# Kernel optimization log

Hardware: AMD Instinct MI355X
Metric: run time of the kernel (lower is better)

Reference implementation:

```python
import jax, jax.numpy as jnp
import numpy as np

B, L = 16, 8192
D, NB, N, NC = 128, 6, 32, 16   # d_model, n_blocks, complex state modes (d_state//2), num_classes
E = 2 * D                       # FF expansion (expand=2)


def setup_inputs() -> dict:
    key = jax.random.key(0)
    ks = jax.random.split(key, 16)
    rn = lambda k, s, sc=0.02: jax.random.normal(k, s, jnp.float32) * sc
    return {
        "x": jax.random.normal(ks[0], (B, L, 1), jnp.float32),
        "conv_w": rn(ks[1], (D, 1, 5), 0.3),
        "conv_b": jnp.zeros((D,), jnp.float32),
        "s4_ln_w": jnp.ones((NB, D), jnp.float32),
        "s4_ln_b": jnp.zeros((NB, D), jnp.float32),
        "s4_log_dt": jax.random.uniform(ks[2], (NB, D), jnp.float32, np.log(1e-3), np.log(1e-1)),
        "s4_log_A_real": jnp.full((NB, D, N), np.log(0.5), jnp.float32),
        "s4_A_imag": jnp.ones((NB, D, 1), jnp.float32) * (np.pi * jnp.arange(N, dtype=jnp.float32)),
        "s4_C_re": rn(ks[3], (NB, D, N), 1.0),
        "s4_C_im": rn(ks[4], (NB, D, N), 1.0),
        "s4_D": rn(ks[5], (NB, D), 1.0),
        "s4_out_w": rn(ks[6], (NB, 2 * D, D)),
        "s4_out_b": jnp.zeros((NB, 2 * D), jnp.float32),
        "ff_ln_w": jnp.ones((NB, D), jnp.float32),
        "ff_ln_b": jnp.zeros((NB, D), jnp.float32),
        "ff_w1": rn(ks[7], (NB, E, D)),
        "ff_b1": jnp.zeros((NB, E), jnp.float32),
        "ff_w2": rn(ks[8], (NB, D, E)),
        "ff_b2": jnp.zeros((NB, D), jnp.float32),
        "head_w": rn(ks[9], (NC, D)),
        "head_b": jnp.zeros((NC,), jnp.float32),
    }


def _ln_c(h, w, b):
    # LayerNorm over channel dim of [B, D, L] (prenorm of ResidualBlock, transposed layout)
    mu = h.mean(1, keepdims=True)
    var = ((h - mu) ** 2).mean(1, keepdims=True)
    return (h - mu) * jax.lax.rsqrt(var + 1e-5) * w[None, :, None] + b[None, :, None]


def _s4(z, log_dt, log_A_real, A_imag, C_re, C_im, Dskip, out_w, out_b):
    # S4D diagonal SSM: ZOH-discretized kernel, FFT causal conv, GELU, GLU output projection
    Lq = z.shape[-1]
    dt = jnp.exp(log_dt)                                 # [D]
    A = -jnp.exp(log_A_real) + 1j * A_imag               # [D,N] stable diagonal
    dtA = dt[:, None] * A                                # [D,N]
    C = (C_re + 1j * C_im) * (jnp.exp(dtA) - 1.0) / A    # ZOH input discretization folded into C
    vand = jnp.exp(dtA[:, :, None] * jnp.arange(Lq))     # [D,N,L] Vandermonde of exp(dtA)
    K = 2.0 * jnp.einsum('dn,dnl->dl', C, vand).real     # [D,L] SSM convolution kernel
    nf = 2 * Lq
    y = jnp.fft.irfft(jnp.fft.rfft(z, n=nf) * jnp.fft.rfft(K, n=nf)[None], n=nf)[..., :Lq]
    y = jax.nn.gelu(y + Dskip[None, :, None] * z)        # skip term D*u then activation
    y = jnp.einsum('ed,bdl->bel', out_w, y) + out_b[None, :, None]  # position-wise d->2d
    a, g = jnp.split(y, 2, axis=1)
    return a * jax.nn.sigmoid(g)                          # GLU


def _logits(x, conv_w, conv_b, s4_ln_w, s4_ln_b, s4_log_dt, s4_log_A_real, s4_A_imag, s4_C_re, s4_C_im, s4_D, s4_out_w, s4_out_b, ff_ln_w, ff_ln_b, ff_w1, ff_b1, ff_w2, ff_b2, head_w, head_b):
    u = x.transpose(0, 2, 1)                             # [B,1,L]
    h = jax.lax.conv_general_dilated(u, conv_w, (1,), [(2, 2)], dimension_numbers=('NCH', 'OIH', 'NCH'))
    h = h + conv_b[None, :, None]                        # [B,D,L]
    nb = s4_log_dt.shape[0]
    for i in range(nb):
        z = _ln_c(h, s4_ln_w[i], s4_ln_b[i])
        h = h + _s4(z, s4_log_dt[i], s4_log_A_real[i], s4_A_imag[i], s4_C_re[i], s4_C_im[i], s4_D[i], s4_out_w[i], s4_out_b[i])
        z = _ln_c(h, ff_ln_w[i], ff_ln_b[i])
        z = jax.nn.gelu(jnp.einsum('ed,bdl->bel', ff_w1[i], z) + ff_b1[i][None, :, None])
        h = h + jnp.einsum('de,bel->bdl', ff_w2[i], z) + ff_b2[i][None, :, None]
    last = h[:, :, -1]                                   # take final timestep
    return last @ head_w.T + head_b                      # [B,NC]


def reference(x, conv_w, conv_b, s4_ln_w, s4_ln_b, s4_log_dt, s4_log_A_real, s4_A_imag, s4_C_re, s4_C_im, s4_D, s4_out_w, s4_out_b, ff_ln_w, ff_ln_b, ff_w1, ff_b1, ff_w2, ff_b2, head_w, head_b):
    logits = _logits(x, conv_w, conv_b, s4_ln_w, s4_ln_b, s4_log_dt, s4_log_A_real, s4_A_imag, s4_C_re, s4_C_im, s4_D, s4_out_w, s4_out_b, ff_ln_w, ff_ln_b, ff_w1, ff_b1, ff_w2, ff_b2, head_w, head_b)
    return jnp.argmax(logits, axis=-1)[:, None].astype(jnp.int32)
```

## Files before the change

### kernel.cpp

```cpp
#include <hip/hip_runtime.h>
#include <math.h>

#define Bb 16
#define Ls 8192
#define Dm 128
#define NBK 6
#define Nst 32
#define NCl 16
#define Em 256
#define LC 128
#define NCH 64
#define BL (Bb*Ls)

typedef __attribute__((ext_vector_type(8))) short bfrag;
typedef __attribute__((ext_vector_type(4))) float f32x4;

__device__ __forceinline__ float geluf(float x) {
    float t = x * x;
    float g = x * fmaf(0.102952207f, t, 2.30234547f);
    float e = exp2f(-g);
    return x * __builtin_amdgcn_rcpf(1.f + e);
}
__device__ __forceinline__ float sigmf(float x) {
    return __builtin_amdgcn_rcpf(1.f + exp2f(-1.44269504f * x));
}

__device__ __forceinline__ unsigned short bf16r(float x) {
    unsigned u = __float_as_uint(x);
    return (unsigned short)((u + 0x7FFFu + ((u >> 16) & 1u)) >> 16);
}
__device__ __forceinline__ void split2(float x, unsigned short& h, unsigned short& l) {
    h = bf16r(x);
    float hf = __uint_as_float(((unsigned)h) << 16);
    l = bf16r(x - hf);
}

__global__ void s4e_conv(const float* __restrict__ x, const float* __restrict__ cw,
                         const float* __restrict__ cb, float* __restrict__ h) {
    int tid = blockIdx.x * 256 + threadIdx.x;
    int d4 = tid & 31;
    int t = tid >> 5;
    int l = t & (Ls - 1);
    int b = t >> 13;
    const float* xb = x + (size_t)b * Ls;
    float xs[5];
#pragma unroll
    for (int k = 0; k < 5; ++k) {
        int p = l + k - 2;
        xs[k] = (p >= 0 && p < Ls) ? xb[p] : 0.f;
    }
    float4 acc;
    float* ap = &acc.x;
#pragma unroll
    for (int j = 0; j < 4; ++j) {
        int d = d4 * 4 + j;
        float a = cb[d];
#pragma unroll
        for (int k = 0; k < 5; ++k) a = fmaf(cw[d * 5 + k], xs[k], a);
        ap[j] = a;
    }
    *(float4*)&h[(size_t)t * Dm + d4 * 4] = acc;
}

__global__ void s4e_lnstat(const float* __restrict__ h, float2* __restrict__ stats) {
    int tid = threadIdx.x;
    int t = blockIdx.x * 64 + (tid >> 2);
    int sub = tid & 3;
    const float* hp = h + (size_t)t * Dm + sub * 32;
    float s = 0.f, q = 0.f;
#pragma unroll
    for (int i = 0; i < 8; ++i) {
        float4 v = *(const float4*)(hp + i * 4);
        s += v.x + v.y + v.z + v.w;
        q += v.x * v.x + v.y * v.y + v.z * v.z + v.w * v.w;
    }
    s += __shfl_xor(s, 1); s += __shfl_xor(s, 2);
    q += __shfl_xor(q, 1); q += __shfl_xor(q, 2);
    float mu = s * (1.f / Dm);
    float rs = rsqrtf(q * (1.f / Dm) - mu * mu + 1e-5f);
    if (sub == 0) stats[t] = make_float2(mu, rs);
}

__global__ void s4e_setup6(const float* __restrict__ log_dt, const float* __restrict__ lAr,
                           const float* __restrict__ Aim, const float* __restrict__ Cre,
                           const float* __restrict__ Cim, float2* __restrict__ wv6,
                           float2* __restrict__ wp6, float2* __restrict__ Cc6) {
    int i = blockIdx.x;
    int d = threadIdx.x;
    const float* ld  = log_dt + i * Dm;
    const float* la  = lAr + i * Dm * Nst;
    const float* ai  = Aim + i * Dm * Nst;
    const float* cre = Cre + i * Dm * Nst;
    const float* cim = Cim + i * Dm * Nst;
    float2* wv = wv6 + i * (Nst * Dm);
    float2* wp = wp6 + i * (Nst * Dm);
    float2* Cc = Cc6 + i * (Nst * Dm);
    float dt = expf(ld[d]);
    for (int n = 0; n < Nst; ++n) {
        int id = d * Nst + n;
        float Ar = -expf(la[id]);
        float Ai = ai[id];
        float xr = dt * Ar, xi = dt * Ai;
        float er = expf(xr);
        float wr = er * cosf(xi), wi = er * sinf(xi);
        wv[n * Dm + d] = make_float2(wr, wi);
        float den = Ar * Ar + Ai * Ai;
        float inv = 1.f / den;
        float fr = ((wr - 1.f) * Ar + wi * Ai) * inv;
        float fi = (wi * Ar - (wr - 1.f) * Ai) * inv;
        Cc[n * Dm + d] = make_float2(2.f * (cre[id] * fr - cim[id] * fi),
                                     2.f * (cre[id] * fi + cim[id] * fr));
        float pr = wr, pi = wi;
#pragma unroll
        for (int sq = 0; sq < 7; ++sq) {
            float nr = pr * pr - pi * pi;
            float ni = 2.f * pr * pi;
            pr = nr; pi = ni;
        }
        wp[n * Dm + d] = make_float2(pr, pi);
    }
}

__global__ void s4e_wsplit6(const float* __restrict__ ow, const float* __restrict__ w1,
                            const float* __restrict__ w2, unsigned short* __restrict__ base0) {
    int idx = blockIdx.x * 256 + threadIdx.x;
    int layer = idx / 12288;
    int r = idx - layer * 12288;
    int mat = r >> 12;
    int g = r & 4095;
    int lane = g & 63;
    int fid = g >> 6;
    int col = lane & 15, q = lane >> 4;
    unsigned short* base = base0 + layer * 196608;
    const float* src;
    unsigned short *dh, *dl_;
    int rt, kt, K;
    if (mat == 0)      { src = ow + layer * 32768; K = 128; dh = base;          dl_ = base + 32768;  rt = fid >> 2; kt = fid & 3; }
    else if (mat == 1) { src = w1 + layer * 32768; K = 128; dh = base + 65536;  dl_ = base + 98304;  rt = fid >> 2; kt = fid & 3; }
    else               { src = w2 + layer * 32768; K = 256; dh = base + 131072; dl_ = base + 163840; rt = fid >> 3; kt = fid & 7; }
    int row = rt * 16 + col;
    int k0 = kt * 32 + q * 8;
    const float* sp = src + row * K + k0;
    bfrag vh, vl;
#pragma unroll
    for (int j = 0; j < 8; ++j) {
        unsigned short hh, ll;
        split2(sp[j], hh, ll);
        vh[j] = (short)hh; vl[j] = (short)ll;
    }
    *(bfrag*)&dh[g * 8] = vh;
    *(bfrag*)&dl_[g * 8] = vl;
}

__global__ __launch_bounds__(256) void s4e_s1(const float* __restrict__ h,
        const float2* __restrict__ stats, const float* __restrict__ lnw,
        const float* __restrict__ lnb, const float2* __restrict__ wv,
        float2* __restrict__ send) {
    __shared__ float2 stl[LC];
    int tid = threadIdx.x;
    int blk = blockIdx.x;
    int half = blk & 1;
    int chunk = blk >> 1;
    int c = chunk & (NCH - 1);
    int b = chunk >> 6;
    int dl = tid & 15;
    int m  = (tid >> 4) & 3;
    int dq = tid >> 6;
    int d  = half * 64 + dq * 16 + dl;
    int n0 = m * 8;
    if (tid < LC) stl[tid] = stats[(size_t)b * Ls + c * LC + tid];
    float wr[8], wi[8], sr[8], si[8];
#pragma unroll
    for (int k = 0; k < 8; ++k) {
        float2 t = wv[(n0 + k) * Dm + d];
        wr[k] = t.x; wi[k] = t.y; sr[k] = 0.f; si[k] = 0.f;
    }
    float wd = lnw[d], bd = lnb[d];
    const float* hp = h + ((size_t)b * Ls + c * LC) * Dm + d;
    __syncthreads();
#pragma unroll 1
    for (int j = 0; j < LC; j += 4) {
        float hv[4];
#pragma unroll
        for (int u = 0; u < 4; ++u) hv[u] = hp[(size_t)(j + u) * Dm];
        float zv[4];
#pragma unroll
        for (int u = 0; u < 4; ++u) {
            float2 sj = stl[j + u];
            zv[u] = (hv[u] - sj.x) * sj.y * wd + bd;
        }
#pragma unroll
        for (int u = 0; u < 4; ++u) {
            float z = zv[u];
#pragma unroll
            for (int k = 0; k < 8; ++k) {
                float t = fmaf(-wi[k], si[k], z);
                float nr = fmaf(wr[k], sr[k], t);
                float ni = fmaf(wi[k], sr[k], wr[k] * si[k]);
                sr[k] = nr; si[k] = ni;
            }
        }
    }
    float2* o = send + ((size_t)(b * NCH + c) * Nst + n0) * Dm + d;
#pragma unroll
    for (int k = 0; k < 8; ++k) o[k * Dm] = make_float2(sr[k], si[k]);
}

__global__ void s4e_s2(const float2* __restrict__ wp, float2* __restrict__ s) {
    int tid = blockIdx.x * 256 + threadIdx.x;
    int d = tid & 127;
    int n = (tid >> 7) & 31;
    int b = tid >> 12;
    float2 W = wp[n * Dm + d];
    float Sr = 0.f, Si = 0.f;
    size_t base = ((size_t)(b * NCH) * Nst + n) * Dm + d;
    size_t cs = (size_t)Nst * Dm;
    for (int c0 = 0; c0 < NCH; c0 += 8) {
        float2 E[8];
#pragma unroll
        for (int k = 0; k < 8; ++k) E[k] = s[base + (size_t)(c0 + k) * cs];
#pragma unroll
        for (int k = 0; k < 8; ++k) {
            float2 o = make_float2(Sr, Si);
            float nr = fmaf(W.x, Sr, fmaf(-W.y, Si, E[k].x));
            float ni = fmaf(W.x, Si, fmaf(W.y, Sr, E[k].y));
            Sr = nr; Si = ni;
            s[base + (size_t)(c0 + k) * cs] = o;
        }
    }
}

__global__ __launch_bounds__(256) void s4e_s3(const float* __restrict__ h,
        const float2* __restrict__ stats, const float* __restrict__ lnw,
        const float* __restrict__ lnb, const float2* __restrict__ wv,
        const float2* __restrict__ Cc, const float2* __restrict__ sinit,
        const float* __restrict__ Dsk,
        unsigned short* __restrict__ acth, unsigned short* __restrict__ actl) {
    __shared__ float2 stl[LC];
    int tid = threadIdx.x;
    int blk = blockIdx.x;
    int half = blk & 1;
    int chunk = blk >> 1;
    int c = chunk & (NCH - 1);
    int b = chunk >> 6;
    int dl = tid & 15;
    int m  = (tid >> 4) & 3;
    int dq = tid >> 6;
    int d  = half * 64 + dq * 16 + dl;
    int n0 = m * 8;
    if (tid < LC) stl[tid] = stats[(size_t)b * Ls + c * LC + tid];
    float wr[8], wi[8], cr[8], ci[8], sr[8], si[8];
    const float2* s0 = sinit + ((size_t)(b * NCH + c) * Nst + n0) * Dm + d;
#pragma unroll
    for (int k = 0; k < 8; ++k) {
        float2 t = wv[(n0 + k) * Dm + d];  wr[k] = t.x; wi[k] = t.y;
        float2 cc = Cc[(n0 + k) * Dm + d]; cr[k] = cc.x; ci[k] = cc.y;
        float2 ss = s0[k * Dm];            sr[k] = ss.x; si[k] = ss.y;
    }
    float wd = lnw[d], bd = lnb[d];
    float Dv = Dsk[d];
    size_t ib = ((size_t)b * Ls + c * LC) * Dm + d;
    __syncthreads();
#pragma unroll 1
    for (int j = 0; j < LC; j += 4) {
        float hv[4];
#pragma unroll
        for (int u = 0; u < 4; ++u) hv[u] = h[ib + (size_t)(j + u) * Dm];
        float zv[4];
#pragma unroll
        for (int u = 0; u < 4; ++u) {
            float2 sj = stl[j + u];
            zv[u] = (hv[u] - sj.x) * sj.y * wd + bd;
        }
#pragma unroll
        for (int u = 0; u < 4; ++u) {
            float z = zv[u];
            float acc = 0.f;
#pragma unroll
            for (int k = 0; k < 8; ++k) {
                float t = fmaf(-wi[k], si[k], z);
                float nr = fmaf(wr[k], sr[k], t);
                float ni = fmaf(wi[k], sr[k], wr[k] * si[k]);
                sr[k] = nr; si[k] = ni;
                acc = fmaf(cr[k], nr, acc);
                acc = fmaf(-ci[k], ni, acc);
            }
            acc += __shfl_xor(acc, 16);
            acc += __shfl_xor(acc, 32);
            if (m == 0) {
                float av = geluf(fmaf(Dv, z, acc));
                unsigned short hh, ll;
                split2(av, hh, ll);
                acth[ib + (size_t)(j + u) * Dm] = hh;
                actl[ib + (size_t)(j + u) * Dm] = ll;
            }
        }
    }
}

__global__ __launch_bounds__(256) void s4e_outproj(const unsigned short* __restrict__ acth,
        const unsigned short* __restrict__ actl, const unsigned short* __restrict__ wsp,
        const float* __restrict__ bias, float* __restrict__ h) {
    __shared__ __align__(16) unsigned short smem[8192];
    unsigned short* Ah = smem;
    unsigned short* Al = smem + 4096;
    float* Rf = (float*)smem;
    const unsigned short* Whi = wsp;
    const unsigned short* Wlo = wsp + 32768;
    size_t l0 = (size_t)blockIdx.x * 32;
    int tid = threadIdx.x;
    {
        const unsigned short* gh = acth + l0 * Dm;
        const unsigned short* gl = actl + l0 * Dm;
        for (int i = tid * 8; i < 32 * 128; i += 2048) {
            int r = i >> 7;
            int di = i ^ ((r & 7) << 3);
            *(bfrag*)&Ah[di] = *(const bfrag*)&gh[i];
            *(bfrag*)&Al[di] = *(const bfrag*)&gl[i];
        }
    }
    __syncthreads();
    int w = tid >> 6, lane = tid & 63;
    int col = lane & 15, q = lane >> 4;
    f32x4 acc[2][4];
#pragma unroll
    for (int m = 0; m < 2; ++m)
#pragma unroll
        for (int nt = 0; nt < 4; ++nt) acc[m][nt] = (f32x4){0.f, 0.f, 0.f, 0.f};
#pragma unroll
    for (int ks = 0; ks < 4; ++ks) {
        int kb = ks * 32 + q * 8;
        int i0 = (col * 128 + kb) ^ ((col & 7) << 3);
        int i1 = ((16 + col) * 128 + kb) ^ ((col & 7) << 3);
        bfrag a0h = *(bfrag*)&Ah[i0], a0l = *(bfrag*)&Al[i0];
        bfrag a1h = *(bfrag*)&Ah[i1], a1l = *(bfrag*)&Al[i1];
#pragma unroll
        for (int nt = 0; nt < 4; ++nt) {
            int rt = (nt < 2) ? (w * 2 + nt) : (8 + w * 2 + (nt - 2));
            int off = ((rt * 4 + ks) * 64 + lane) * 8;
            bfrag bh = *(const bfrag*)&Whi[off];
            bfrag bl = *(const bfrag*)&Wlo[off];
            acc[0][nt] = __builtin_amdgcn_mfma_f32_16x16x32_bf16(a0h, bh, acc[0][nt], 0, 0, 0);
            acc[0][nt] = __builtin_amdgcn_mfma_f32_16x16x32_bf16(a0h, bl, acc[0][nt], 0, 0, 0);
            acc[0][nt] = __builtin_amdgcn_mfma_f32_16x16x32_bf16(a0l, bh, acc[0][nt], 0, 0, 0);
            acc[1][nt] = __builtin_amdgcn_mfma_f32_16x16x32_bf16(a1h, bh, acc[1][nt], 0, 0, 0);
            acc[1][nt] = __builtin_amdgcn_mfma_f32_16x16x32_bf16(a1h, bl, acc[1][nt], 0, 0, 0);
            acc[1][nt] = __builtin_amdgcn_mfma_f32_16x16x32_bf16(a1l, bh, acc[1][nt], 0, 0, 0);
        }
    }
    __syncthreads();
#pragma unroll
    for (int m = 0; m < 2; ++m)
#pragma unroll
        for (int nt = 0; nt < 2; ++nt) {
            int dout = w * 32 + nt * 16 + col;
            float ba = bias[dout], bg = bias[dout + 128];
#pragma unroll
            for (int r = 0; r < 4; ++r) {
                int l = m * 16 + q * 4 + r;
                float a = acc[m][nt][r] + ba;
                float g = acc[m][nt + 2][r] + bg;
                Rf[l * 128 + dout] = a * sigmf(g);
            }
        }
    __syncthreads();
    size_t gb = l0 * Dm + (size_t)tid * 16;
#pragma unroll
    for (int i = 0; i < 4; ++i) {
        float4 r = *(float4*)&Rf[tid * 16 + i * 4];
        float4 hv = *(float4*)&h[gb + i * 4];
        hv.x += r.x; hv.y += r.y; hv.z += r.z; hv.w += r.w;
        *(float4*)&h[gb + i * 4] = hv;
    }
}

__global__ __launch_bounds__(256) void s4e_ffk(const float* __restrict__ lnw,
        const float* __restrict__ lnb, const unsigned short* __restrict__ wsp,
        const float* __restrict__ b1, const float* __restrict__ b2, float* __restrict__ h) {
    __shared__ __align__(16) unsigned short smem[24576];
    unsigned short* Zh = smem;
    unsigned short* Zl = smem + 4096;
    unsigned short* Eh = smem + 8192;
    unsigned short* El = smem + 16384;
    float* Rf = (float*)smem;
    const unsigned short* W1h = wsp + 65536;
    const unsigned short* W1l = wsp + 98304;
    const unsigned short* W2h = wsp + 131072;
    const unsigned short* W2l = wsp + 163840;
    size_t l0 = (size_t)blockIdx.x * 32;
    int tid = threadIdx.x;
    float hf[16];
    float s = 0.f, qq = 0.f;
    {
        const float* hp = h + l0 * Dm + (size_t)tid * 16;
#pragma unroll
        for (int i = 0; i < 4; ++i) {
            float4 v = *(const float4*)(hp + i * 4);
            hf[i * 4 + 0] = v.x; hf[i * 4 + 1] = v.y;
            hf[i * 4 + 2] = v.z; hf[i * 4 + 3] = v.w;
            s += v.x + v.y + v.z + v.w;
            qq += v.x * v.x + v.y * v.y + v.z * v.z + v.w * v.w;
        }
    }
    s  += __shfl_xor(s, 1);  s += __shfl_xor(s, 2);  s += __shfl_xor(s, 4);
    qq += __shfl_xor(qq, 1); qq += __shfl_xor(qq, 2); qq += __shfl_xor(qq, 4);
    float mu = s * (1.f / Dm);
    float rs = rsqrtf(qq * (1.f / Dm) - mu * mu + 1e-5f);
    int tok = tid >> 3, dc = (tid & 7) * 16;
#pragma unroll
    for (int g = 0; g < 2; ++g) {
        bfrag vh, vl;
#pragma unroll
        for (int k = 0; k < 8; ++k) {
            int d = dc + g * 8 + k;
            float v = (hf[g * 8 + k] - mu) * rs * lnw[d] + lnb[d];
            unsigned short hh, ll;
            split2(v, hh, ll);
            vh[k] = (short)hh; vl[k] = (short)ll;
        }
        int idx = (tok * 128 + dc + g * 8) ^ ((tok & 7) << 3);
        *(bfrag*)&Zh[idx] = vh;
        *(bfrag*)&Zl[idx] = vl;
    }
    __syncthreads();
    int w = tid >> 6, lane = tid & 63;
    int col = lane & 15, q = lane >> 4;
    f32x4 acc[2][4];
#pragma unroll
    for (int m = 0; m < 2; ++m)
#pragma unroll
        for (int nt = 0; nt < 4; ++nt) acc[m][nt] = (f32x4){0.f, 0.f, 0.f, 0.f};
#pragma unroll
    for (int ks = 0; ks < 4; ++ks) {
        int kb = ks * 32 + q * 8;
        int i0 = (col * 128 + kb) ^ ((col & 7) << 3);
        int i1 = ((16 + col) * 128 + kb) ^ ((col & 7) << 3);
        bfrag a0h = *(bfrag*)&Zh[i0], a0l = *(bfrag*)&Zl[i0];
        bfrag a1h = *(bfrag*)&Zh[i1], a1l = *(bfrag*)&Zl[i1];
#pragma unroll
        for (int nt = 0; nt < 4; ++nt) {
            int rt = w * 4 + nt;
            int off = ((rt * 4 + ks) * 64 + lane) * 8;
            bfrag bh = *(const bfrag*)&W1h[off];
            bfrag bl = *(const bfrag*)&W1l[off];
            acc[0][nt] = __builtin_amdgcn_mfma_f32_16x16x32_bf16(a0h, bh, acc[0][nt], 0, 0, 0);
            acc[0][nt] = __builtin_amdgcn_mfma_f32_16x16x32_bf16(a0h, bl, acc[0][nt], 0, 0, 0);
            acc[0][nt] = __builtin_amdgcn_mfma_f32_16x16x32_bf16(a0l, bh, acc[0][nt], 0, 0, 0);
            acc[1][nt] = __builtin_amdgcn_mfma_f32_16x16x32_bf16(a1h, bh, acc[1][nt], 0, 0, 0);
            acc[1][nt] = __builtin_amdgcn_mfma_f32_16x16x32_bf16(a1h, bl, acc[1][nt], 0, 0, 0);
            acc[1][nt] = __builtin_amdgcn_mfma_f32_16x16x32_bf16(a1l, bh, acc[1][nt], 0, 0, 0);
        }
    }
#pragma unroll
    for (int m = 0; m < 2; ++m)
#pragma unroll
        for (int nt = 0; nt < 4; ++nt) {
            int ei = w * 64 + nt * 16 + col;
            float bv = b1[ei];
#pragma unroll
            for (int r = 0; r < 4; ++r) {
                int l = m * 16 + q * 4 + r;
                float v = geluf(acc[m][nt][r] + bv);
                unsigned short hh, ll;
                split2(v, hh, ll);
                int idx = (l * 256 + ei) ^ ((l & 7) << 3);
                Eh[idx] = hh; El[idx] = ll;
            }
        }
    __syncthreads();
    f32x4 acc2[2][2];
#pragma unroll
    for (int m = 0; m < 2; ++m)
#pragma unroll
        for (int nt = 0; nt < 2; ++nt) acc2[m][nt] = (f32x4){0.f, 0.f, 0.f, 0.f};
#pragma unroll
    for (int ks = 0; ks < 8; ++ks) {
        int kb = ks * 32 + q * 8;
        int i0 = (col * 256 + kb) ^ ((col & 7) << 3);
        int i1 = ((16 + col) * 256 + kb) ^ ((col & 7) << 3);
        bfrag a0h = *(bfrag*)&Eh[i0], a0l = *(bfrag*)&El[i0];
        bfrag a1h = *(bfrag*)&Eh[i1], a1l = *(bfrag*)&El[i1];
#pragma unroll
        for (int nt = 0; nt < 2; ++nt) {
            int rt = w * 2 + nt;
            int off = ((rt * 8 + ks) * 64 + lane) * 8;
            bfrag bh = *(const bfrag*)&W2h[off];
            bfrag bl = *(const bfrag*)&W2l[off];
            acc2[0][nt] = __builtin_amdgcn_mfma_f32_16x16x32_bf16(a0h, bh, acc2[0][nt], 0, 0, 0);
            acc2[0][nt] = __builtin_amdgcn_mfma_f32_16x16x32_bf16(a0h, bl, acc2[0][nt], 0, 0, 0);
            acc2[0][nt] = __builtin_amdgcn_mfma_f32_16x16x32_bf16(a0l, bh, acc2[0][nt], 0, 0, 0);
            acc2[1][nt] = __builtin_amdgcn_mfma_f32_16x16x32_bf16(a1h, bh, acc2[1][nt], 0, 0, 0);
            acc2[1][nt] = __builtin_amdgcn_mfma_f32_16x16x32_bf16(a1h, bl, acc2[1][nt], 0, 0, 0);
            acc2[1][nt] = __builtin_amdgcn_mfma_f32_16x16x32_bf16(a1l, bh, acc2[1][nt], 0, 0, 0);
        }
    }
#pragma unroll
    for (int m = 0; m < 2; ++m)
#pragma unroll
        for (int nt = 0; nt < 2; ++nt) {
            int dout = w * 32 + nt * 16 + col;
            float bv = b2[dout];
#pragma unroll
            for (int r = 0; r < 4; ++r) {
                int l = m * 16 + q * 4 + r;
                Rf[l * 128 + dout] = acc2[m][nt][r] + bv;
            }
        }
    __syncthreads();
    size_t gb = l0 * Dm + (size_t)tid * 16;
#pragma unroll
    for (int i = 0; i < 4; ++i) {
        float4 r = *(float4*)&Rf[tid * 16 + i * 4];
        float4 o;
        o.x = hf[i * 4 + 0] + r.x; o.y = hf[i * 4 + 1] + r.y;
        o.z = hf[i * 4 + 2] + r.z; o.w = hf[i * 4 + 3] + r.w;
        *(float4*)&h[gb + i * 4] = o;
    }
}

__global__ void s4e_head(const float* __restrict__ h, const float* __restrict__ hw,
                         const float* __restrict__ hb, int* __restrict__ out) {
    __shared__ float logit[Bb][NCl];
    int tid = threadIdx.x;
    int b = tid >> 4, c = tid & 15;
    const float* hp = h + ((size_t)b * Ls + (Ls - 1)) * Dm;
    float acc = hb[c];
    for (int d = 0; d < Dm; ++d) acc = fmaf(hp[d], hw[c * Dm + d], acc);
    logit[b][c] = acc;
    __syncthreads();
    if (c == 0) {
        float best = logit[b][0]; int bi = 0;
#pragma unroll
        for (int k = 1; k < NCl; ++k) {
            float v = logit[b][k];
            if (v > best) { best = v; bi = k; }
        }
        out[b] = bi;
    }
}

extern "C" void kernel_launch(void* const* d_in, const int* in_sizes, int n_in,
                              void* d_out, int out_size, void* d_ws, size_t ws_size,
                              hipStream_t stream) {
    const float* x        = (const float*)d_in[0];
    const float* conv_w   = (const float*)d_in[1];
    const float* conv_b   = (const float*)d_in[2];
    const float* s4_ln_w  = (const float*)d_in[3];
    const float* s4_ln_b  = (const float*)d_in[4];
    const float* s4_logdt = (const float*)d_in[5];
    const float* s4_lAr   = (const float*)d_in[6];
    const float* s4_Aim   = (const float*)d_in[7];
    const float* s4_Cre   = (const float*)d_in[8];
    const float* s4_Cim   = (const float*)d_in[9];
    const float* s4_D     = (const float*)d_in[10];
    const float* s4_ow    = (const float*)d_in[11];
    const float* s4_ob    = (const float*)d_in[12];
    const float* ff_ln_w  = (const float*)d_in[13];
    const float* ff_ln_b  = (const float*)d_in[14];
    const float* ff_w1    = (const float*)d_in[15];
    const float* ff_b1    = (const float*)d_in[16];
    const float* ff_w2    = (const float*)d_in[17];
    const float* ff_b2    = (const float*)d_in[18];
    const float* head_w   = (const float*)d_in[19];
    const float* head_b   = (const float*)d_in[20];
    int* out = (int*)d_out;

    float* ws = (float*)d_ws;
    float* h  = ws;
    float2* stats = (float2*)(ws + 16777216);
    float2* wv6 = (float2*)(ws + 17039360);
    float2* wp6 = (float2*)(ws + 17088512);
    float2* Cc6 = (float2*)(ws + 17137664);
    unsigned short* wsp6 = (unsigned short*)(ws + 17186816);
    unsigned short* acth = (unsigned short*)(ws + 33554432);
    unsigned short* actl = (unsigned short*)(ws + 41943040);
    float2* send  = (float2*)(ws + 50331648);

    s4e_conv<<<BL * 32 / 256, 256, 0, stream>>>(x, conv_w, conv_b, h);
    s4e_setup6<<<NBK, 128, 0, stream>>>(s4_logdt, s4_lAr, s4_Aim, s4_Cre, s4_Cim,
                                        wv6, wp6, Cc6);
    s4e_wsplit6<<<288, 256, 0, stream>>>(s4_ow, ff_w1, ff_w2, wsp6);
    for (int i = 0; i < NBK; ++i) {
        float2* wv = wv6 + i * (Nst * Dm);
        float2* wp = wp6 + i * (Nst * Dm);
        float2* Cc = Cc6 + i * (Nst * Dm);
        unsigned short* wsp = wsp6 + i * 196608;
        s4e_lnstat<<<BL / 64, 256, 0, stream>>>(h, stats);
        s4e_s1<<<2048, 256, 0, stream>>>(h, stats, s4_ln_w + i * Dm, s4_ln_b + i * Dm, wv, send);
        s4e_s2<<<256, 256, 0, stream>>>(wp, send);
        s4e_s3<<<2048, 256, 0, stream>>>(h, stats, s4_ln_w + i * Dm, s4_ln_b + i * Dm,
                                         wv, Cc, send, s4_D + i * Dm, acth, actl);
        s4e_outproj<<<BL / 32, 256, 0, stream>>>(acth, actl, wsp, s4_ob + i * Em, h);
        s4e_ffk<<<BL / 32, 256, 0, stream>>>(ff_ln_w + i * Dm, ff_ln_b + i * Dm, wsp,
                                             ff_b1 + i * Em, ff_b2 + i * Dm, h);
    }
    s4e_head<<<1, 256, 0, stream>>>(h, head_w, head_b, out);
}
```

Baseline: 2.153 ms.

## Fuse LayerNorm stats into conv and FF epilogues; widen s3 per-thread state modes

The separate LayerNorm-statistics kernel is removed. The conv kernel and the feed-forward kernel epilogue now compute per-timestep mean and rstd while writing h, which saves a full read of h before each block. Separately, the s3 scan kernel gives each thread 16 state modes instead of 8 and covers all 128 channels in one block. This halves the grid and drops one shuffle reduction, at the cost of more registers and less parallelism. The stats written by the ffk epilogue for the next block assume each group of 8 threads covers one timestep's 128 channels.

```diff
diff --git a/kernel.cpp b/kernel.cpp
--- a/kernel.cpp
+++ b/kernel.cpp
@@ -36,7 +36,8 @@
 }
 
 __global__ void s4e_conv(const float* __restrict__ x, const float* __restrict__ cw,
-                         const float* __restrict__ cb, float* __restrict__ h) {
+                         const float* __restrict__ cb, float* __restrict__ h,
+                         float2* __restrict__ stats) {
     int tid = blockIdx.x * 256 + threadIdx.x;
     int d4 = tid & 31;
     int t = tid >> 5;
@@ -60,25 +61,18 @@
         ap[j] = a;
     }
     *(float4*)&h[(size_t)t * Dm + d4 * 4] = acc;
-}
-
-__global__ void s4e_lnstat(const float* __restrict__ h, float2* __restrict__ stats) {
-    int tid = threadIdx.x;
-    int t = blockIdx.x * 64 + (tid >> 2);
-    int sub = tid & 3;
-    const float* hp = h + (size_t)t * Dm + sub * 32;
-    float s = 0.f, q = 0.f;
-#pragma unroll
-    for (int i = 0; i < 8; ++i) {
-        float4 v = *(const float4*)(hp + i * 4);
-        s += v.x + v.y + v.z + v.w;
-        q += v.x * v.x + v.y * v.y + v.z * v.z + v.w * v.w;
-    }
-    s += __shfl_xor(s, 1); s += __shfl_xor(s, 2);
-    q += __shfl_xor(q, 1); q += __shfl_xor(q, 2);
-    float mu = s * (1.f / Dm);
-    float rs = rsqrtf(q * (1.f / Dm) - mu * mu + 1e-5f);
-    if (sub == 0) stats[t] = make_float2(mu, rs);
+    float s = acc.x + acc.y + acc.z + acc.w;
+    float q = acc.x * acc.x + acc.y * acc.y + acc.z * acc.z + acc.w * acc.w;
+    s += __shfl_xor(s, 1);  q += __shfl_xor(q, 1);
+    s += __shfl_xor(s, 2);  q += __shfl_xor(q, 2);
+    s += __shfl_xor(s, 4);  q += __shfl_xor(q, 4);
+    s += __shfl_xor(s, 8);  q += __shfl_xor(q, 8);
+    s += __shfl_xor(s, 16); q += __shfl_xor(q, 16);
+    if (d4 == 0) {
+        float mu = s * (1.f / Dm);
+        float rs = rsqrtf(q * (1.f / Dm) - mu * mu + 1e-5f);
+        stats[t] = make_float2(mu, rs);
+    }
 }
 
 __global__ void s4e_setup6(const float* __restrict__ log_dt, const float* __restrict__ lAr,
@@ -239,20 +233,18 @@
     __shared__ float2 stl[LC];
     int tid = threadIdx.x;
     int blk = blockIdx.x;
-    int half = blk & 1;
-    int chunk = blk >> 1;
-    int c = chunk & (NCH - 1);
-    int b = chunk >> 6;
-    int dl = tid & 15;
-    int m  = (tid >> 4) & 3;
-    int dq = tid >> 6;
-    int d  = half * 64 + dq * 16 + dl;
-    int n0 = m * 8;
+    int c = blk & (NCH - 1);
+    int b = blk >> 6;
+    int dl = tid & 31;
+    int m  = (tid >> 5) & 1;
+    int dh = tid >> 6;
+    int d  = dh * 32 + dl;
+    int n0 = m * 16;
     if (tid < LC) stl[tid] = stats[(size_t)b * Ls + c * LC + tid];
-    float wr[8], wi[8], cr[8], ci[8], sr[8], si[8];
+    float wr[16], wi[16], cr[16], ci[16], sr[16], si[16];
     const float2* s0 = sinit + ((size_t)(b * NCH + c) * Nst + n0) * Dm + d;
 #pragma unroll
-    for (int k = 0; k < 8; ++k) {
+    for (int k = 0; k < 16; ++k) {
         float2 t = wv[(n0 + k) * Dm + d];  wr[k] = t.x; wi[k] = t.y;
         float2 cc = Cc[(n0 + k) * Dm + d]; cr[k] = cc.x; ci[k] = cc.y;
         float2 ss = s0[k * Dm];            sr[k] = ss.x; si[k] = ss.y;
@@ -277,7 +269,7 @@
             float z = zv[u];
             float acc = 0.f;
 #pragma unroll
-            for (int k = 0; k < 8; ++k) {
+            for (int k = 0; k < 16; ++k) {
                 float t = fmaf(-wi[k], si[k], z);
                 float nr = fmaf(wr[k], sr[k], t);
                 float ni = fmaf(wi[k], sr[k], wr[k] * si[k]);
@@ -285,7 +277,6 @@
                 acc = fmaf(cr[k], nr, acc);
                 acc = fmaf(-ci[k], ni, acc);
             }
-            acc += __shfl_xor(acc, 16);
             acc += __shfl_xor(acc, 32);
             if (m == 0) {
                 float av = geluf(fmaf(Dv, z, acc));
@@ -376,7 +367,8 @@
 
 __global__ __launch_bounds__(256) void s4e_ffk(const float* __restrict__ lnw,
         const float* __restrict__ lnb, const unsigned short* __restrict__ wsp,
-        const float* __restrict__ b1, const float* __restrict__ b2, float* __restrict__ h) {
+        const float* __restrict__ b1, const float* __restrict__ b2, float* __restrict__ h,
+        float2* __restrict__ stats) {
     __shared__ __align__(16) unsigned short smem[24576];
     unsigned short* Zh = smem;
     unsigned short* Zl = smem + 4096;
@@ -508,6 +500,7 @@
         }
     __syncthreads();
     size_t gb = l0 * Dm + (size_t)tid * 16;
+    float s2_ = 0.f, q2_ = 0.f;
 #pragma unroll
     for (int i = 0; i < 4; ++i) {
         float4 r = *(float4*)&Rf[tid * 16 + i * 4];
@@ -515,6 +508,16 @@
         o.x = hf[i * 4 + 0] + r.x; o.y = hf[i * 4 + 1] + r.y;
         o.z = hf[i * 4 + 2] + r.z; o.w = hf[i * 4 + 3] + r.w;
         *(float4*)&h[gb + i * 4] = o;
+        s2_ += o.x + o.y + o.z + o.w;
+        q2_ += o.x * o.x + o.y * o.y + o.z * o.z + o.w * o.w;
+    }
+    s2_ += __shfl_xor(s2_, 1); q2_ += __shfl_xor(q2_, 1);
+    s2_ += __shfl_xor(s2_, 2); q2_ += __shfl_xor(q2_, 2);
+    s2_ += __shfl_xor(s2_, 4); q2_ += __shfl_xor(q2_, 4);
+    if ((tid & 7) == 0) {
+        float mu2 = s2_ * (1.f / Dm);
+        float rs2 = rsqrtf(q2_ * (1.f / Dm) - mu2 * mu2 + 1e-5f);
+        stats[l0 + (tid >> 3)] = make_float2(mu2, rs2);
     }
 }
 
@@ -576,7 +579,7 @@
     unsigned short* actl = (unsigned short*)(ws + 41943040);
     float2* send  = (float2*)(ws + 50331648);
 
-    s4e_conv<<<BL * 32 / 256, 256, 0, stream>>>(x, conv_w, conv_b, h);
+    s4e_conv<<<BL * 32 / 256, 256, 0, stream>>>(x, conv_w, conv_b, h, stats);
     s4e_setup6<<<NBK, 128, 0, stream>>>(s4_logdt, s4_lAr, s4_Aim, s4_Cre, s4_Cim,
                                         wv6, wp6, Cc6);
     s4e_wsplit6<<<288, 256, 0, stream>>>(s4_ow, ff_w1, ff_w2, wsp6);
@@ -585,14 +588,13 @@
         float2* wp = wp6 + i * (Nst * Dm);
         float2* Cc = Cc6 + i * (Nst * Dm);
         unsigned short* wsp = wsp6 + i * 196608;
-        s4e_lnstat<<<BL / 64, 256, 0, stream>>>(h, stats);
         s4e_s1<<<2048, 256, 0, stream>>>(h, stats, s4_ln_w + i * Dm, s4_ln_b + i * Dm, wv, send);
         s4e_s2<<<256, 256, 0, stream>>>(wp, send);
-        s4e_s3<<<2048, 256, 0, stream>>>(h, stats, s4_ln_w + i * Dm, s4_ln_b + i * Dm,
+        s4e_s3<<<1024, 256, 0, stream>>>(h, stats, s4_ln_w + i * Dm, s4_ln_b + i * Dm,
                                          wv, Cc, send, s4_D + i * Dm, acth, actl);
         s4e_outproj<<<BL / 32, 256, 0, stream>>>(acth, actl, wsp, s4_ob + i * Em, h);
         s4e_ffk<<<BL / 32, 256, 0, stream>>>(ff_ln_w + i * Dm, ff_ln_b + i * Dm, wsp,
-                                             ff_b1 + i * Em, ff_b2 + i * Dm, h);
+                                             ff_b1 + i * Em, ff_b2 + i * Dm, h, stats);
     }
     s4e_head<<<1, 256, 0, stream>>>(h, head_w, head_b, out);
 }
```

Result: faster. 1.968 ms (-8.6%).
